# Performance work log

Measured on AMD Instinct MI355X. Metric: run time of the kernel, lower is better.

## Reference

```python
import jax, jax.numpy as jnp
import numpy as np

B, S, E, H = 4, 2048, 1024, 16
DH = E // H
NEG = -1e11


def setup_inputs() -> dict:
    key = jax.random.key(0)
    ks = jax.random.split(key, 9)
    scale = 1.0 / np.sqrt(E)
    return {
        "x": jax.random.normal(ks[0], (B, S, E), jnp.float32),
        "Wq": jax.random.normal(ks[1], (E, E), jnp.float32) * scale,
        "bq": jnp.zeros((E,), jnp.float32),
        "Wk": jax.random.normal(ks[2], (E, E), jnp.float32) * scale,
        "bk": jnp.zeros((E,), jnp.float32),
        "Wv": jax.random.normal(ks[3], (E, E), jnp.float32) * scale,
        "bv": jnp.zeros((E,), jnp.float32),
        "Wo": jax.random.normal(ks[4], (E, E), jnp.float32) * scale,
        "bo": jnp.zeros((E,), jnp.float32),
    }


def reference(x, Wq, bq, Wk, bk, Wv, bv, Wo, bo):
    # Faithful to the TF code: split_heads uses a pure reshape (B,S,E)->(B,H,S,DH),
    # which interleaves positions/features rather than transposing heads.
    def split_heads(e):
        return jnp.reshape(e, (-1, H, S, DH))

    q = split_heads(x @ Wq + bq)
    k = split_heads(x @ Wk + bk)
    v = split_heads(x @ Wv + bv)
    # scores: [B, H, S, S]
    w = jnp.einsum("bhqd,bhkd->bhqk", q, k) / np.sqrt(DH)
    mask = jnp.triu(jnp.ones((1, 1, S, S), jnp.float32), 1) * NEG
    w = w + mask
    w = jax.nn.softmax(w, axis=-1)
    z = jnp.einsum("bhqk,bhkd->bhqd", w, v)
    z = jnp.reshape(z, (-1, S, E))
    return z @ Wo + bo
```

## Files before the change

### kernel.cpp

```cpp
#include <hip/hip_runtime.h>
#include <hip/hip_bf16.h>

typedef unsigned short u16;
typedef __attribute__((ext_vector_type(8))) short bf16x8;
typedef __attribute__((ext_vector_type(4))) float f32x4;
typedef __attribute__((ext_vector_type(8))) unsigned short u16x8;
typedef __attribute__((ext_vector_type(4))) unsigned int u32x4;

#define MFMA16(a, b, c) __builtin_amdgcn_mfma_f32_16x16x32_bf16((a), (b), (c), 0, 0, 0)

#define SWZB(row) ((((row) & 3) | ((((row) >> 3) & 1) << 2)) << 4)

__device__ __forceinline__ u16 f2b(float f) {
  union { float f; unsigned u; } c; c.f = f;
  unsigned u = c.u;
  u += 0x7FFFu + ((u >> 16) & 1u);
  return (u16)(u >> 16);
}

__device__ __forceinline__ unsigned cvt_pk_bf16(float a, float b) {
  unsigned r;
  asm("v_cvt_pk_bf16_f32 %0, %1, %2" : "=v"(r) : "v"(a), "v"(b));
  return r;
}

__device__ __forceinline__ void gload_lds16(const u16* g, u16* l) {
  __builtin_amdgcn_global_load_lds(
      (__attribute__((address_space(1))) void*)(g),
      (__attribute__((address_space(3))) void*)(l),
      16, 0, 0);
}

__global__ __launch_bounds__(256) void convert_f32_bf16(const float* __restrict__ in,
                                                        u16* __restrict__ out) {
  int i = (blockIdx.x * 256 + threadIdx.x) * 8;
  float4 a = *(const float4*)&in[i];
  float4 b = *(const float4*)&in[i + 4];
  u16x8 o;
  o[0] = f2b(a.x); o[1] = f2b(a.y); o[2] = f2b(a.z); o[3] = f2b(a.w);
  o[4] = f2b(b.x); o[5] = f2b(b.y); o[6] = f2b(b.z); o[7] = f2b(b.w);
  *(u16x8*)&out[i] = o;
}

__global__ __launch_bounds__(256) void transpose_convert_w(
    const float* __restrict__ W0, const float* __restrict__ W1,
    const float* __restrict__ W2, const float* __restrict__ W3,
    u16* __restrict__ Wts) {
  __shared__ float t[32][33];
  int z = blockIdx.z;
  const float* W = (z == 0) ? W0 : (z == 1) ? W1 : (z == 2) ? W2 : W3;
  u16* Wt = Wts + (size_t)z * 1048576;
  int n0 = blockIdx.x * 32, k0 = blockIdx.y * 32;
  int tx = threadIdx.x, ty = threadIdx.y;
#pragma unroll
  for (int i = 0; i < 32; i += 8)
    t[ty + i][tx] = W[(size_t)(k0 + ty + i) * 1024 + n0 + tx];
  __syncthreads();
#pragma unroll
  for (int i = 0; i < 32; i += 8)
    Wt[(size_t)(n0 + ty + i) * 1024 + k0 + tx] = f2b(t[tx][ty + i]);
}

__global__ __launch_bounds__(256) void transpose_v(const u16* __restrict__ V,
                                                   u16* __restrict__ Vt) {
  __shared__ u16 t[32][33];
  int bh = blockIdx.z;
  int s0 = blockIdx.x * 32, d0 = blockIdx.y * 32;
  const u16* Vb = V + (size_t)bh * 131072;
  u16* Vtb = Vt + (size_t)bh * 131072;
  int tx = threadIdx.x, ty = threadIdx.y;
#pragma unroll
  for (int i = 0; i < 32; i += 8)
    t[ty + i][tx] = Vb[(s0 + ty + i) * 64 + d0 + tx];
  __syncthreads();
#pragma unroll
  for (int i = 0; i < 32; i += 8)
    Vtb[(d0 + ty + i) * 2048 + s0 + tx] = t[tx][ty + i];
}

template <bool F32OUT>
__global__ __launch_bounds__(256) void gemm_kernel(
    const u16* __restrict__ A, const u16* __restrict__ Wt0,
    const float* __restrict__ bias0, const float* __restrict__ bias1,
    const float* __restrict__ bias2,
    u16* __restrict__ outB, float* __restrict__ outF) {
  int z = blockIdx.z;
  const u16* Wt = Wt0 + (size_t)z * 1048576;
  const float* bias = (z == 0) ? bias0 : (z == 1) ? bias1 : bias2;
  u16* outb = outB + (size_t)z * 8388608;
  float oscale = (!F32OUT && z == 0) ? 0.125f * 1.44269504088896f : 1.0f;

  __shared__ u16 Alds[128 * 32];
  __shared__ u16 Blds[128 * 32];
  int tid = threadIdx.x;
  int lane = tid & 63, w = tid >> 6;
  int brow = blockIdx.x * 128;
  int bcol = blockIdx.y * 128;
  int wr = (w >> 1) * 64, wc = (w & 1) * 64;
  int r = lane & 15, half = lane >> 4;

  f32x4 acc[4][4] = {};
  int f0 = (w * 2 + 0) * 512 + lane * 8;
  int f1 = (w * 2 + 1) * 512 + lane * 8;
  const u16* Abase = A + (size_t)brow * 1024;
  const u16* Bbase = Wt + (size_t)bcol * 1024;

  for (int k0 = 0; k0 < 1024; k0 += 32) {
    gload_lds16(Abase + (size_t)(f0 >> 5) * 1024 + k0 + (f0 & 31), &Alds[(w * 2 + 0) * 512]);
    gload_lds16(Abase + (size_t)(f1 >> 5) * 1024 + k0 + (f1 & 31), &Alds[(w * 2 + 1) * 512]);
    gload_lds16(Bbase + (size_t)(f0 >> 5) * 1024 + k0 + (f0 & 31), &Blds[(w * 2 + 0) * 512]);
    gload_lds16(Bbase + (size_t)(f1 >> 5) * 1024 + k0 + (f1 & 31), &Blds[(w * 2 + 1) * 512]);
    __syncthreads();
    bf16x8 af[4], bf[4];
#pragma unroll
    for (int m = 0; m < 4; ++m)
      af[m] = *(const bf16x8*)&Alds[(wr + m * 16 + r) * 32 + half * 8];
#pragma unroll
    for (int n = 0; n < 4; ++n)
      bf[n] = *(const bf16x8*)&Blds[(wc + n * 16 + r) * 32 + half * 8];
#pragma unroll
    for (int m = 0; m < 4; ++m)
#pragma unroll
      for (int n = 0; n < 4; ++n)
        acc[m][n] = MFMA16(af[m], bf[n], acc[m][n]);
    __syncthreads();
  }
#pragma unroll
  for (int m = 0; m < 4; ++m) {
    int rowb = brow + wr + m * 16 + half * 4;
#pragma unroll
    for (int n = 0; n < 4; ++n) {
      int col = bcol + wc + n * 16 + r;
      float bv = bias[col];
#pragma unroll
      for (int j = 0; j < 4; ++j) {
        float v = (acc[m][n][j] + bv) * oscale;
        size_t idx = (size_t)(rowb + j) * 1024 + col;
        if (F32OUT) outF[idx] = v;
        else        outb[idx] = f2b(v);
      }
    }
  }
}

__device__ __forceinline__ void attn_stage(
    const u16* __restrict__ Kb, const u16* __restrict__ Vtb,
    u16* Kl, u16* Vl, int kb, int tid) {
  const int row0 = tid >> 3;
  const int cb0 = (tid & 7) << 4;
  const int row1 = row0 + 32;
  gload_lds16(Kb + (size_t)(kb + row0) * 64 + ((cb0 ^ SWZB(row0)) >> 1), Kl + tid * 8);
  gload_lds16(Kb + (size_t)(kb + row1) * 64 + ((cb0 ^ SWZB(row1)) >> 1), Kl + 2048 + tid * 8);
  gload_lds16(Vtb + (size_t)row0 * 2048 + kb + ((cb0 ^ SWZB(row0)) >> 1), Vl + tid * 8);
  gload_lds16(Vtb + (size_t)row1 * 2048 + kb + ((cb0 ^ SWZB(row1)) >> 1), Vl + 2048 + tid * 8);
}

__device__ __forceinline__ void attn_strip(
    const u16* __restrict__ Qb, const u16* __restrict__ Kb,
    const u16* __restrict__ Vtb, u16* __restrict__ Zb,
    u16 (*Kl)[4096], u16 (*Vl)[4096], int qrow, int nt, int tid) {
  const int lane = tid & 63;
  const int r = lane & 15, half = lane >> 4;
  const bf16x8 qf0 = *(const bf16x8*)&Qb[(qrow + r) * 64 + half * 8];
  const bf16x8 qf1 = *(const bf16x8*)&Qb[(qrow + r) * 64 + 32 + half * 8];
  const int q = qrow + r;
  f32x4 om[4] = {};
  float m_run = -1e30f, l_run = 0.f;

  __syncthreads();
  attn_stage(Kb, Vtb, Kl[0], Vl[0], 0, tid);
  int cur = 0;

  for (int kt = 0; kt < nt; ++kt) {
    const int kb = kt * 64;
    __syncthreads();
    if (kt + 1 < nt) attn_stage(Kb, Vtb, Kl[cur ^ 1], Vl[cur ^ 1], kb + 64, tid);
    const char* Kc = (const char*)Kl[cur];
    const char* Vc = (const char*)Vl[cur];

    f32x4 sT[2][2];
#pragma unroll
    for (int c = 0; c < 2; ++c)
#pragma unroll
      for (int t = 0; t < 2; ++t) {
        const int krow = c * 32 + ((r >> 2) << 3) + t * 4 + (r & 3);
        const char* krp = Kc + krow * 128;
        const bf16x8 kf0 = *(const bf16x8*)(krp + ((half * 16) ^ SWZB(krow)));
        const bf16x8 kf1 = *(const bf16x8*)(krp + ((64 + half * 16) ^ SWZB(krow)));
        f32x4 zacc = {};
        zacc = MFMA16(kf0, qf0, zacc);
        zacc = MFMA16(kf1, qf1, zacc);
        sT[c][t] = zacc;
      }
    if (kt == nt - 1) {
#pragma unroll
      for (int c = 0; c < 2; ++c)
#pragma unroll
        for (int t = 0; t < 2; ++t)
#pragma unroll
          for (int j = 0; j < 4; ++j)
            if (kb + c * 32 + half * 8 + t * 4 + j > q) sT[c][t][j] = -1e30f;
    }
    float mloc;
    {
      float a0 = fmaxf(fmaxf(sT[0][0][0], sT[0][0][1]), fmaxf(sT[0][0][2], sT[0][0][3]));
      float a1 = fmaxf(fmaxf(sT[0][1][0], sT[0][1][1]), fmaxf(sT[0][1][2], sT[0][1][3]));
      float a2 = fmaxf(fmaxf(sT[1][0][0], sT[1][0][1]), fmaxf(sT[1][0][2], sT[1][0][3]));
      float a3 = fmaxf(fmaxf(sT[1][1][0], sT[1][1][1]), fmaxf(sT[1][1][2], sT[1][1][3]));
      mloc = fmaxf(fmaxf(a0, a1), fmaxf(a2, a3));
    }
    mloc = fmaxf(mloc, __shfl_xor(mloc, 16));
    mloc = fmaxf(mloc, __shfl_xor(mloc, 32));
    if (__any(mloc > m_run + 8.0f)) {
      const float nm = fmaxf(m_run, mloc);
      const float corr = __builtin_exp2f(m_run - nm);
      m_run = nm;
      l_run *= corr;
#pragma unroll
      for (int f = 0; f < 4; ++f)
#pragma unroll
        for (int j = 0; j < 4; ++j) om[f][j] *= corr;
    }
    const float mb = m_run;
    float lloc = 0.f;
    u32x4 pw[2];
#pragma unroll
    for (int c = 0; c < 2; ++c)
#pragma unroll
      for (int t = 0; t < 2; ++t) {
        const float e0 = __builtin_exp2f(sT[c][t][0] - mb);
        const float e1 = __builtin_exp2f(sT[c][t][1] - mb);
        const float e2 = __builtin_exp2f(sT[c][t][2] - mb);
        const float e3 = __builtin_exp2f(sT[c][t][3] - mb);
        lloc += (e0 + e1) + (e2 + e3);
        pw[c][t * 2 + 0] = cvt_pk_bf16(e0, e1);
        pw[c][t * 2 + 1] = cvt_pk_bf16(e2, e3);
      }
    lloc += __shfl_xor(lloc, 16);
    lloc += __shfl_xor(lloc, 32);
    l_run += lloc;
#pragma unroll
    for (int c = 0; c < 2; ++c) {
      const bf16x8 pb = __builtin_bit_cast(bf16x8, pw[c]);
#pragma unroll
      for (int f = 0; f < 4; ++f) {
        const int vrow = f * 16 + r;
        const bf16x8 vf = *(const bf16x8*)(Vc + vrow * 128 + ((c * 64 + half * 16) ^ SWZB(vrow)));
        om[f] = MFMA16(vf, pb, om[f]);
      }
    }
    cur ^= 1;
  }
  const float inv = 1.0f / l_run;
#pragma unroll
  for (int f = 0; f < 4; ++f) {
    ushort4 st;
    st.x = f2b(om[f][0] * inv);
    st.y = f2b(om[f][1] * inv);
    st.z = f2b(om[f][2] * inv);
    st.w = f2b(om[f][3] * inv);
    *(ushort4*)&Zb[(size_t)q * 64 + f * 16 + half * 4] = st;
  }
}

__global__ __launch_bounds__(256) void attn_kernel(
    const u16* __restrict__ Q, const u16* __restrict__ K,
    const u16* __restrict__ Vt, u16* __restrict__ Z) {
  __shared__ u16 Kl[2][4096];
  __shared__ u16 Vl[2][4096];
  const int L = blockIdx.x;
  const int xcd = L & 7;
  const int i = L >> 3;
  const int bh = ((i >> 4) << 3) + xcd;
  const int x = i & 15;
  const int tid = threadIdx.x;
  const int w = tid >> 6;
  const u16* Qb = Q + (size_t)bh * 131072;
  const u16* Kb = K + (size_t)bh * 131072;
  const u16* Vb = Vt + (size_t)bh * 131072;
  u16* Zb = Z + (size_t)bh * 131072;
  attn_strip(Qb, Kb, Vb, Zb, Kl, Vl, x * 64 + w * 16, x + 1, tid);
  attn_strip(Qb, Kb, Vb, Zb, Kl, Vl, (31 - x) * 64 + w * 16, 32 - x, tid);
}

extern "C" void kernel_launch(void* const* d_in, const int* in_sizes, int n_in,
                              void* d_out, int out_size, void* d_ws, size_t ws_size,
                              hipStream_t stream) {
  (void)in_sizes; (void)n_in; (void)out_size; (void)ws_size;
  const float* x  = (const float*)d_in[0];
  const float* Wq = (const float*)d_in[1];
  const float* bq = (const float*)d_in[2];
  const float* Wk = (const float*)d_in[3];
  const float* bk = (const float*)d_in[4];
  const float* Wv = (const float*)d_in[5];
  const float* bv = (const float*)d_in[6];
  const float* Wo = (const float*)d_in[7];
  const float* bo = (const float*)d_in[8];
  float* out = (float*)d_out;

  char* ws = (char*)d_ws;
  u16* xb  = (u16*)(ws);
  u16* Wts = (u16*)(ws + 16777216);
  u16* Qb  = (u16*)(ws + 25165824);
  u16* Kb  = (u16*)(ws + 41943040);
  u16* Vb  = (u16*)(ws + 58720256);
  u16* Vtb = (u16*)(ws + 75497472);

  convert_f32_bf16<<<4096, 256, 0, stream>>>(x, xb);
  {
    dim3 g(32, 32, 4), b(32, 8);
    transpose_convert_w<<<g, b, 0, stream>>>(Wq, Wk, Wv, Wo, Wts);
  }
  {
    dim3 g(64, 8, 3), b(256);
    gemm_kernel<false><<<g, b, 0, stream>>>(xb, Wts, bq, bk, bv, Qb, nullptr);
  }
  {
    dim3 g(64, 2, 64), b(32, 8);
    transpose_v<<<g, b, 0, stream>>>(Vb, Vtb);
  }
  {
    dim3 g(1024), b(256);
    attn_kernel<<<g, b, 0, stream>>>(Qb, Kb, Vtb, xb );
  }
  {
    dim3 g(64, 8, 1), b(256);
    gemm_kernel<true><<<g, b, 0, stream>>>(xb, Wts + 3 * 1048576, bo, bo, bo, Qb, out);
  }
}
```

Measured before the change: 192.5 us.

## Process two 16-row query tiles per wave in one contiguous attention strip

The attention kernel now gives each block a single contiguous 128-row query strip, with each wave handling 32 rows as two 16-row tiles that share every K/V LDS fragment load. This replaces the earlier scheme of two 64-row strips per block paired for causal load balance. It also precomputes swizzled LDS addresses and moves the per-tile row-sum reduction to the end. It adds s_setprio around MFMA phases and launch_bounds(256,4) for occupancy. Blocks now do unequal work (nt = 2x+2), so the causal load balance may be lost, and the extra accumulators raise register pressure.

```diff
diff --git a/kernel.cpp b/kernel.cpp
--- a/kernel.cpp
+++ b/kernel.cpp
@@ -143,127 +143,58 @@
   }
 }
 
-__device__ __forceinline__ void attn_stage(
-    const u16* __restrict__ Kb, const u16* __restrict__ Vtb,
-    u16* Kl, u16* Vl, int kb, int tid) {
-  const int row0 = tid >> 3;
-  const int cb0 = (tid & 7) << 4;
-  const int row1 = row0 + 32;
-  gload_lds16(Kb + (size_t)(kb + row0) * 64 + ((cb0 ^ SWZB(row0)) >> 1), Kl + tid * 8);
-  gload_lds16(Kb + (size_t)(kb + row1) * 64 + ((cb0 ^ SWZB(row1)) >> 1), Kl + 2048 + tid * 8);
-  gload_lds16(Vtb + (size_t)row0 * 2048 + kb + ((cb0 ^ SWZB(row0)) >> 1), Vl + tid * 8);
-  gload_lds16(Vtb + (size_t)row1 * 2048 + kb + ((cb0 ^ SWZB(row1)) >> 1), Vl + 2048 + tid * 8);
-}
-
-__device__ __forceinline__ void attn_strip(
-    const u16* __restrict__ Qb, const u16* __restrict__ Kb,
-    const u16* __restrict__ Vtb, u16* __restrict__ Zb,
-    u16 (*Kl)[4096], u16 (*Vl)[4096], int qrow, int nt, int tid) {
-  const int lane = tid & 63;
-  const int r = lane & 15, half = lane >> 4;
-  const bf16x8 qf0 = *(const bf16x8*)&Qb[(qrow + r) * 64 + half * 8];
-  const bf16x8 qf1 = *(const bf16x8*)&Qb[(qrow + r) * 64 + 32 + half * 8];
-  const int q = qrow + r;
-  f32x4 om[4] = {};
-  float m_run = -1e30f, l_run = 0.f;
-
-  __syncthreads();
-  attn_stage(Kb, Vtb, Kl[0], Vl[0], 0, tid);
-  int cur = 0;
-
-  for (int kt = 0; kt < nt; ++kt) {
-    const int kb = kt * 64;
-    __syncthreads();
-    if (kt + 1 < nt) attn_stage(Kb, Vtb, Kl[cur ^ 1], Vl[cur ^ 1], kb + 64, tid);
-    const char* Kc = (const char*)Kl[cur];
-    const char* Vc = (const char*)Vl[cur];
-
-    f32x4 sT[2][2];
+__device__ __forceinline__ float fmax16(const f32x4 (&s)[2][2]) {
+  float a0 = fmaxf(fmaxf(s[0][0][0], s[0][0][1]), fmaxf(s[0][0][2], s[0][0][3]));
+  float a1 = fmaxf(fmaxf(s[0][1][0], s[0][1][1]), fmaxf(s[0][1][2], s[0][1][3]));
+  float a2 = fmaxf(fmaxf(s[1][0][0], s[1][0][1]), fmaxf(s[1][0][2], s[1][0][3]));
+  float a3 = fmaxf(fmaxf(s[1][1][0], s[1][1][1]), fmaxf(s[1][1][2], s[1][1][3]));
+  return fmaxf(fmaxf(a0, a1), fmaxf(a2, a3));
+}
+
+__device__ __forceinline__ void softmax_tile(
+    f32x4 (&sT)[2][2], int kb, int qmin, int r, int half,
+    float& m_run, float& l_run, f32x4 (&om)[4], u32x4 (&pw)[2]) {
+  if (kb + 63 > qmin) {
+    const int q = qmin + r;
 #pragma unroll
     for (int c = 0; c < 2; ++c)
 #pragma unroll
-      for (int t = 0; t < 2; ++t) {
-        const int krow = c * 32 + ((r >> 2) << 3) + t * 4 + (r & 3);
-        const char* krp = Kc + krow * 128;
-        const bf16x8 kf0 = *(const bf16x8*)(krp + ((half * 16) ^ SWZB(krow)));
-        const bf16x8 kf1 = *(const bf16x8*)(krp + ((64 + half * 16) ^ SWZB(krow)));
-        f32x4 zacc = {};
-        zacc = MFMA16(kf0, qf0, zacc);
-        zacc = MFMA16(kf1, qf1, zacc);
-        sT[c][t] = zacc;
-      }
-    if (kt == nt - 1) {
-#pragma unroll
-      for (int c = 0; c < 2; ++c)
-#pragma unroll
-        for (int t = 0; t < 2; ++t)
-#pragma unroll
-          for (int j = 0; j < 4; ++j)
-            if (kb + c * 32 + half * 8 + t * 4 + j > q) sT[c][t][j] = -1e30f;
+      for (int t = 0; t < 2; ++t)
+#pragma unroll
+        for (int j = 0; j < 4; ++j)
+          if (kb + c * 32 + half * 8 + t * 4 + j > q) sT[c][t][j] = -1e30f;
+  }
+  const float mloc = fmax16(sT);
+  if (__any(mloc > m_run + 8.0f)) {
+    float mr = fmaxf(mloc, __shfl_xor(mloc, 16));
+    mr = fmaxf(mr, __shfl_xor(mr, 32));
+    const float nm = fmaxf(m_run, mr);
+    const float corr = __builtin_exp2f(m_run - nm);
+    m_run = nm;
+    l_run *= corr;
+#pragma unroll
+    for (int f = 0; f < 4; ++f)
+#pragma unroll
+      for (int j = 0; j < 4; ++j) om[f][j] *= corr;
+  }
+  const float mb = m_run;
+  float ll = 0.f;
+#pragma unroll
+  for (int c = 0; c < 2; ++c)
+#pragma unroll
+    for (int t = 0; t < 2; ++t) {
+      const float e0 = __builtin_exp2f(sT[c][t][0] - mb);
+      const float e1 = __builtin_exp2f(sT[c][t][1] - mb);
+      const float e2 = __builtin_exp2f(sT[c][t][2] - mb);
+      const float e3 = __builtin_exp2f(sT[c][t][3] - mb);
+      ll += (e0 + e1) + (e2 + e3);
+      pw[c][t * 2 + 0] = cvt_pk_bf16(e0, e1);
+      pw[c][t * 2 + 1] = cvt_pk_bf16(e2, e3);
     }
-    float mloc;
-    {
-      float a0 = fmaxf(fmaxf(sT[0][0][0], sT[0][0][1]), fmaxf(sT[0][0][2], sT[0][0][3]));
-      float a1 = fmaxf(fmaxf(sT[0][1][0], sT[0][1][1]), fmaxf(sT[0][1][2], sT[0][1][3]));
-      float a2 = fmaxf(fmaxf(sT[1][0][0], sT[1][0][1]), fmaxf(sT[1][0][2], sT[1][0][3]));
-      float a3 = fmaxf(fmaxf(sT[1][1][0], sT[1][1][1]), fmaxf(sT[1][1][2], sT[1][1][3]));
-      mloc = fmaxf(fmaxf(a0, a1), fmaxf(a2, a3));
-    }
-    mloc = fmaxf(mloc, __shfl_xor(mloc, 16));
-    mloc = fmaxf(mloc, __shfl_xor(mloc, 32));
-    if (__any(mloc > m_run + 8.0f)) {
-      const float nm = fmaxf(m_run, mloc);
-      const float corr = __builtin_exp2f(m_run - nm);
-      m_run = nm;
-      l_run *= corr;
-#pragma unroll
-      for (int f = 0; f < 4; ++f)
-#pragma unroll
-        for (int j = 0; j < 4; ++j) om[f][j] *= corr;
-    }
-    const float mb = m_run;
-    float lloc = 0.f;
-    u32x4 pw[2];
-#pragma unroll
-    for (int c = 0; c < 2; ++c)
-#pragma unroll
-      for (int t = 0; t < 2; ++t) {
-        const float e0 = __builtin_exp2f(sT[c][t][0] - mb);
-        const float e1 = __builtin_exp2f(sT[c][t][1] - mb);
-        const float e2 = __builtin_exp2f(sT[c][t][2] - mb);
-        const float e3 = __builtin_exp2f(sT[c][t][3] - mb);
-        lloc += (e0 + e1) + (e2 + e3);
-        pw[c][t * 2 + 0] = cvt_pk_bf16(e0, e1);
-        pw[c][t * 2 + 1] = cvt_pk_bf16(e2, e3);
-      }
-    lloc += __shfl_xor(lloc, 16);
-    lloc += __shfl_xor(lloc, 32);
-    l_run += lloc;
-#pragma unroll
-    for (int c = 0; c < 2; ++c) {
-      const bf16x8 pb = __builtin_bit_cast(bf16x8, pw[c]);
-#pragma unroll
-      for (int f = 0; f < 4; ++f) {
-        const int vrow = f * 16 + r;
-        const bf16x8 vf = *(const bf16x8*)(Vc + vrow * 128 + ((c * 64 + half * 16) ^ SWZB(vrow)));
-        om[f] = MFMA16(vf, pb, om[f]);
-      }
-    }
-    cur ^= 1;
-  }
-  const float inv = 1.0f / l_run;
-#pragma unroll
-  for (int f = 0; f < 4; ++f) {
-    ushort4 st;
-    st.x = f2b(om[f][0] * inv);
-    st.y = f2b(om[f][1] * inv);
-    st.z = f2b(om[f][2] * inv);
-    st.w = f2b(om[f][3] * inv);
-    *(ushort4*)&Zb[(size_t)q * 64 + f * 16 + half * 4] = st;
-  }
-}
-
-__global__ __launch_bounds__(256) void attn_kernel(
+  l_run += ll;
+}
+
+__global__ __launch_bounds__(256, 4) void attn_kernel(
     const u16* __restrict__ Q, const u16* __restrict__ K,
     const u16* __restrict__ Vt, u16* __restrict__ Z) {
   __shared__ u16 Kl[2][4096];
@@ -271,16 +202,124 @@
   const int L = blockIdx.x;
   const int xcd = L & 7;
   const int i = L >> 3;
-  const int bh = ((i >> 4) << 3) + xcd;
+  const int bh = ((i >> 4) << 3) | xcd;
   const int x = i & 15;
   const int tid = threadIdx.x;
   const int w = tid >> 6;
+  const int lane = tid & 63;
+  const int r = lane & 15, half = lane >> 4;
   const u16* Qb = Q + (size_t)bh * 131072;
   const u16* Kb = K + (size_t)bh * 131072;
-  const u16* Vb = Vt + (size_t)bh * 131072;
+  const u16* Vtb = Vt + (size_t)bh * 131072;
   u16* Zb = Z + (size_t)bh * 131072;
-  attn_strip(Qb, Kb, Vb, Zb, Kl, Vl, x * 64 + w * 16, x + 1, tid);
-  attn_strip(Qb, Kb, Vb, Zb, Kl, Vl, (31 - x) * 64 + w * 16, 32 - x, tid);
+
+  const int qw = x * 128 + w * 32;
+  const int nt = 2 * x + 2;
+
+  const bf16x8 qA0 = *(const bf16x8*)&Qb[(qw + r) * 64 + half * 8];
+  const bf16x8 qA1 = *(const bf16x8*)&Qb[(qw + r) * 64 + 32 + half * 8];
+  const bf16x8 qB0 = *(const bf16x8*)&Qb[(qw + 16 + r) * 64 + half * 8];
+  const bf16x8 qB1 = *(const bf16x8*)&Qb[(qw + 16 + r) * 64 + 32 + half * 8];
+
+  const int krow00 = ((r >> 2) << 3) | (r & 3);
+  const int aK0 = krow00 * 128 + ((half * 16) ^ SWZB(krow00));
+  const int aK1 = krow00 * 128 + ((64 + half * 16) ^ SWZB(krow00));
+  const int aV0 = r * 128 + ((half * 16) ^ SWZB(r));
+  const int aV1 = r * 128 + ((64 + half * 16) ^ SWZB(r));
+
+  const int row0 = tid >> 3, row1 = row0 + 32;
+  const int cb0 = (tid & 7) << 4;
+  const u16* kg0 = Kb + (size_t)row0 * 64 + ((cb0 ^ SWZB(row0)) >> 1);
+  const u16* kg1 = Kb + (size_t)row1 * 64 + ((cb0 ^ SWZB(row1)) >> 1);
+  const u16* vg0 = Vtb + (size_t)row0 * 2048 + ((cb0 ^ SWZB(row0)) >> 1);
+  const u16* vg1 = Vtb + (size_t)row1 * 2048 + ((cb0 ^ SWZB(row1)) >> 1);
+  u16* kd0 = &Kl[0][0] + tid * 8;  u16* kd1 = kd0 + 2048;
+  u16* vd0 = &Vl[0][0] + tid * 8;  u16* vd1 = vd0 + 2048;
+
+  f32x4 omA[4] = {}, omB[4] = {};
+  u32x4 pwA[2], pwB[2];
+  float mA = -1e30f, mB = -1e30f, lA = 0.f, lB = 0.f;
+
+  gload_lds16(kg0, kd0); gload_lds16(kg1, kd1);
+  gload_lds16(vg0, vd0); gload_lds16(vg1, vd1);
+  kg0 += 4096; kg1 += 4096; vg0 += 64; vg1 += 64;
+  int curB = 0;
+
+  for (int kt = 0; kt < nt; ++kt) {
+    const int kb = kt * 64;
+    __syncthreads();
+    if (kt + 1 < nt) {
+      const int nb = curB ^ 8192;
+      gload_lds16(kg0, (u16*)((char*)kd0 + nb));
+      gload_lds16(kg1, (u16*)((char*)kd1 + nb));
+      gload_lds16(vg0, (u16*)((char*)vd0 + nb));
+      gload_lds16(vg1, (u16*)((char*)vd1 + nb));
+      kg0 += 4096; kg1 += 4096; vg0 += 64; vg1 += 64;
+    }
+    const char* Kc = (const char*)&Kl[0][0] + curB;
+    const char* Vc = (const char*)&Vl[0][0] + curB;
+
+    f32x4 sT[2][2];
+    __builtin_amdgcn_s_setprio(1);
+#pragma unroll
+    for (int c = 0; c < 2; ++c)
+#pragma unroll
+      for (int t = 0; t < 2; ++t) {
+        const bf16x8 kf0 = *(const bf16x8*)(Kc + aK0 + c * 4096 + t * 512);
+        const bf16x8 kf1 = *(const bf16x8*)(Kc + aK1 + c * 4096 + t * 512);
+        f32x4 z = {};
+        z = MFMA16(kf0, qA0, z);
+        z = MFMA16(kf1, qA1, z);
+        sT[c][t] = z;
+      }
+    __builtin_amdgcn_s_setprio(0);
+    softmax_tile(sT, kb, qw, r, half, mA, lA, omA, pwA);
+    __builtin_amdgcn_s_setprio(1);
+#pragma unroll
+    for (int c = 0; c < 2; ++c)
+#pragma unroll
+      for (int t = 0; t < 2; ++t) {
+        const bf16x8 kf0 = *(const bf16x8*)(Kc + aK0 + c * 4096 + t * 512);
+        const bf16x8 kf1 = *(const bf16x8*)(Kc + aK1 + c * 4096 + t * 512);
+        f32x4 z = {};
+        z = MFMA16(kf0, qB0, z);
+        z = MFMA16(kf1, qB1, z);
+        sT[c][t] = z;
+      }
+    __builtin_amdgcn_s_setprio(0);
+    softmax_tile(sT, kb, qw + 16, r, half, mB, lB, omB, pwB);
+    __builtin_amdgcn_s_setprio(1);
+#pragma unroll
+    for (int c = 0; c < 2; ++c) {
+      const bf16x8 pa = __builtin_bit_cast(bf16x8, pwA[c]);
+      const bf16x8 pb = __builtin_bit_cast(bf16x8, pwB[c]);
+      const int av = c ? aV1 : aV0;
+#pragma unroll
+      for (int f = 0; f < 4; ++f) {
+        const bf16x8 vf = *(const bf16x8*)(Vc + av + f * 2048);
+        omA[f] = MFMA16(vf, pa, omA[f]);
+        omB[f] = MFMA16(vf, pb, omB[f]);
+      }
+    }
+    __builtin_amdgcn_s_setprio(0);
+    curB ^= 8192;
+  }
+
+  lA += __shfl_xor(lA, 16); lA += __shfl_xor(lA, 32);
+  lB += __shfl_xor(lB, 16); lB += __shfl_xor(lB, 32);
+  const float invA = 1.0f / lA;
+  const float invB = 1.0f / lB;
+  const int qa = qw + r, qb2 = qw + 16 + r;
+#pragma unroll
+  for (int f = 0; f < 4; ++f) {
+    ushort4 sa, sb;
+    sa.x = f2b(omA[f][0] * invA); sa.y = f2b(omA[f][1] * invA);
+    sa.z = f2b(omA[f][2] * invA); sa.w = f2b(omA[f][3] * invA);
+    sb.x = f2b(omB[f][0] * invB); sb.y = f2b(omB[f][1] * invB);
+    sb.z = f2b(omB[f][2] * invB); sb.w = f2b(omB[f][3] * invB);
+    *(ushort4*)&Zb[(size_t)qa * 64 + f * 16 + half * 4] = sa;
+    *(ushort4*)&Zb[(size_t)qb2 * 64 + f * 16 + half * 4] = sb;
+  }
 }
 
 extern "C" void kernel_launch(void* const* d_in, const int* in_sizes, int n_in,
```

Measured after the change: 238.7 us. +24.0%, slower.
